# Kernel optimization log

Hardware: AMD Instinct MI355X
Metric: run time of the kernel (lower is better)

## Reference

```python
import jax, jax.numpy as jnp
import numpy as np

B, T, N, C_IN = 2, 12, 50000, 1
H = 16          # hidden = out channels of STConv
KT = 3          # temporal kernel size
E = 800000      # edges (avg degree 16)
NUM_CLASSES = 2


def _temporal_conv(x, wP, bP, wQ, bQ, wR, bR):
    # Gated temporal conv (GLU): relu(P * sigmoid(Q) + R), 'valid' conv over time.
    # x: (B, Tt, N, C); w*: (KT, C, H)
    Tt = x.shape[1]
    def conv(w, b):
        out = b
        for k in range(KT):  # KT=3, tiny unrolled loop
            out = out + jnp.einsum('btnc,co->btno', x[:, k:Tt - KT + 1 + k], w[k])
        return out
    return jax.nn.relu(conv(wP, bP) * jax.nn.sigmoid(conv(wQ, bQ)) + conv(wR, bR))


def _cheb_conv(x, edge_index, edge_weight, w, b):
    # ChebConv K=2, sym normalization, lambda_max=2:
    #   out  = Tx_0 @ W0 + Tx_1 @ W1 + b
    src, dst = edge_index[0], edge_index[1]
    n = x.shape[2]
    deg = jax.ops.segment_sum(edge_weight, src, num_segments=n)
    dis = jnp.where(deg > 0, jax.lax.rsqrt(jnp.maximum(deg, 1e-12)), 0.0)
    norm = -dis[src] * edge_weight * dis[dst]                    # (E,)
    Bc, Tc, _, Hc = x.shape
    xf = jnp.transpose(x, (2, 0, 1, 3)).reshape(n, -1)           # (N, B*T*H)
    agg = jax.ops.segment_sum(norm[:, None] * xf[src], dst, num_segments=n)
    tx1 = jnp.transpose(agg.reshape(n, Bc, Tc, Hc), (1, 2, 0, 3))  # (B, T, N, H)
    return jnp.einsum('btnc,co->btno', x, w[0]) + jnp.einsum('btnc,co->btno', tx1, w[1]) + b


def _forward(x, edge_index, edge_weight,
             tc1_P_w, tc1_P_b, tc1_Q_w, tc1_Q_b, tc1_R_w, tc1_R_b,
             cheb_w, cheb_b,
             tc2_P_w, tc2_P_b, tc2_Q_w, tc2_Q_b, tc2_R_w, tc2_R_b,
             lin_w, lin_b):
    h = _temporal_conv(x, tc1_P_w, tc1_P_b, tc1_Q_w, tc1_Q_b, tc1_R_w, tc1_R_b)  # (B, T-2, N, H)
    h = jax.nn.relu(_cheb_conv(h, edge_index, edge_weight, cheb_w, cheb_b))
    h = _temporal_conv(h, tc2_P_w, tc2_P_b, tc2_Q_w, tc2_Q_b, tc2_R_w, tc2_R_b)  # (B, T-4, N, H)
    h = h.mean(axis=1)                                                            # (B, N, H)
    return h @ lin_w + lin_b                                                      # (B, N, classes)


def setup_inputs() -> dict:
    key = jax.random.key(0)
    ks = jax.random.split(key, 12)
    x = jax.random.normal(ks[0], (B, T, N, C_IN), jnp.float32)
    edge_index = jax.random.randint(ks[1], (2, E), 0, N, dtype=jnp.int32).astype(jnp.int64)
    edge_weight = jax.random.uniform(ks[2], (E,), jnp.float32)

    def conv_w(k, cin, cout):
        s = 1.0 / np.sqrt(cin * KT)
        return jax.random.uniform(k, (KT, cin, cout), jnp.float32, -s, s)

    inp = {'x': x, 'edge_index': edge_index, 'edge_weight': edge_weight}
    for i, name in enumerate(['tc1_P', 'tc1_Q', 'tc1_R']):
        inp[name + '_w'] = conv_w(ks[3 + i], C_IN, H)
        inp[name + '_b'] = jnp.zeros((H,), jnp.float32)
    for i, name in enumerate(['tc2_P', 'tc2_Q', 'tc2_R']):
        inp[name + '_w'] = conv_w(ks[6 + i], H, H)
        inp[name + '_b'] = jnp.zeros((H,), jnp.float32)
    sc = 1.0 / np.sqrt(H)
    inp['cheb_w'] = jax.random.uniform(ks[9], (2, H, H), jnp.float32, -sc, sc)
    inp['cheb_b'] = jnp.zeros((H,), jnp.float32)
    inp['lin_w'] = jax.random.uniform(ks[10], (H, NUM_CLASSES), jnp.float32, -sc, sc)
    inp['lin_b'] = jnp.zeros((NUM_CLASSES,), jnp.float32)
    return inp


def reference(x, edge_index, edge_weight,
              tc1_P_w, tc1_P_b, tc1_Q_w, tc1_Q_b, tc1_R_w, tc1_R_b,
              tc2_P_w, tc2_P_b, tc2_Q_w, tc2_Q_b, tc2_R_w, tc2_R_b,
              cheb_w, cheb_b, lin_w, lin_b):
    return _forward(x, edge_index, edge_weight,
                    tc1_P_w, tc1_P_b, tc1_Q_w, tc1_Q_b, tc1_R_w, tc1_R_b,
                    cheb_w, cheb_b,
                    tc2_P_w, tc2_P_b, tc2_Q_w, tc2_Q_b, tc2_R_w, tc2_R_b,
                    lin_w, lin_b)
```

## Files before the change

kernel.cpp:

```cpp
#include <hip/hip_runtime.h>

typedef unsigned short ushort_t;
typedef unsigned int uint_t;

constexpr int Bb = 2, Tt = 12, Nn = 50000, Hh = 16, Ee = 800000;
constexpr int T1 = 10, T2 = 8;
constexpr int F = 320;
constexpr int NP = 50176;
constexpr int CAP = 64;

#define DEV __device__ __forceinline__

DEV float bf2f(ushort_t u) { return __uint_as_float(((uint_t)u) << 16); }
DEV ushort_t f2bf(float f) {
  uint_t u = __float_as_uint(f);
  u += 0x7fffu + ((u >> 16) & 1u);
  return (ushort_t)(u >> 16);
}
DEV float blo(uint_t u) { return __uint_as_float(u << 16); }
DEV float bhi(uint_t u) { return __uint_as_float(u & 0xffff0000u); }
DEV float sigm(float x) { return 1.0f / (1.0f + __expf(-x)); }

DEV float loadF(const void* p, int j, int isb) {
  return isb ? bf2f(((const ushort_t*)p)[j]) : ((const float*)p)[j];
}
DEV int loadI(const void* p, long long j, int is64) {
  return is64 ? (int)(((const long long*)p)[j]) : ((const int*)p)[j];
}

__global__ void k_wprep(const void* ew, const void* ei,
                        const void* t1Pw, const void* t1Pb,
                        const void* t1Qw, const void* t1Qb,
                        const void* t1Rw, const void* t1Rb,
                        const void* t2Pw, const void* t2Pb,
                        const void* t2Qw, const void* t2Qb,
                        const void* t2Rw, const void* t2Rb,
                        const void* chw, const void* chb,
                        const void* lw, const void* lb,
                        int* flags, float* W, uint_t* zero_base) {
  int gid = blockIdx.x * 256 + threadIdx.x;
  if (gid < 9 * NP) zero_base[gid] = 0u;
  if (blockIdx.x != 0) return;

  __shared__ int sflags[2];
  int tid = threadIdx.x;
  if (tid < 64) {
    int lane = tid;
    const ushort_t* u = (const ushort_t*)ew;
    int cnt = 0;
    for (int j = lane; j < 512; j += 64) cnt += (u[j] < 0x3F80u) ? 1 : 0;
#pragma unroll
    for (int d = 32; d; d >>= 1) cnt += __shfl_xor(cnt, d, 64);
    const int* e32 = (const int*)ei;
    int even_nz = 0, odd_nz = 0;
    for (int j = 2 * lane; j < 256; j += 128) {
      even_nz |= (e32[j] != 0);
      odd_nz |= (e32[j + 1] != 0);
    }
    unsigned long long be = __ballot(even_nz), bo = __ballot(odd_nz);
    if (lane == 0) {
      int f0 = (cnt >= 450) ? 1 : 0;
      int f1 = (bo == 0ull && be != 0ull) ? 1 : 0;
      sflags[0] = f0; sflags[1] = f1;
      flags[0] = f0; flags[1] = f1;
    }
  }
  __syncthreads();
  int isb = sflags[0];
#define CVT(src, off, n) for (int j = tid; j < (n); j += 256) W[(off) + j] = loadF(src, j, isb);
  CVT(t1Pw, 0, 48)   CVT(t1Pb, 48, 16)
  CVT(t1Qw, 64, 48)  CVT(t1Qb, 112, 16)
  CVT(t1Rw, 128, 48) CVT(t1Rb, 176, 16)
  CVT(t2Pw, 192, 768)  CVT(t2Pb, 960, 16)
  CVT(t2Qw, 976, 768)  CVT(t2Qb, 1744, 16)
  CVT(t2Rw, 1760, 768) CVT(t2Rb, 2528, 16)
  CVT(chw, 2544, 512)  CVT(chb, 3056, 16)
  CVT(lw, 3072, 32)    CVT(lb, 3104, 2)
#undef CVT
}

__global__ __launch_bounds__(256) void k_pre(const void* __restrict__ x,
                                             const void* __restrict__ ei,
                                             const void* __restrict__ ew,
                                             const float* __restrict__ W,
                                             const int* __restrict__ flags,
                                             ushort_t* __restrict__ xfh,
                                             float* __restrict__ deg8,
                                             int* __restrict__ cnt,
                                             int2* __restrict__ ecv) {
  int id = blockIdx.x * 256 + threadIdx.x;
  int isb = flags[0];
  if (id < Ee) {
    int is64 = flags[1];
    int s = loadI(ei, id, is64), d = loadI(ei, (long long)Ee + id, is64);
    float w = loadF(ew, id, isb);
    atomicAdd(&deg8[(blockIdx.x & 7) * NP + s], w);
    int pos = atomicAdd(&cnt[d], 1);
    if (pos < CAP) ecv[d * CAP + pos] = make_int2(s, __float_as_int(w));
  }
  if (id < Bb * T1 * Nn) {
    int n = id % Nn;
    int bt = id / Nn;
    int t = bt % T1, b = bt / T1;
    float x0 = loadF(x, (b * Tt + t + 0) * Nn + n, isb);
    float x1 = loadF(x, (b * Tt + t + 1) * Nn + n, isb);
    float x2 = loadF(x, (b * Tt + t + 2) * Nn + n, isb);
    ushort_t g[16];
#pragma unroll
    for (int h = 0; h < 16; ++h) {
      float p = W[48 + h] + x0 * W[0 + h] + x1 * W[16 + h] + x2 * W[32 + h];
      float q = W[112 + h] + x0 * W[64 + h] + x1 * W[80 + h] + x2 * W[96 + h];
      float r = W[176 + h] + x0 * W[128 + h] + x1 * W[144 + h] + x2 * W[160 + h];
      g[h] = f2bf(fmaxf(fmaf(p, sigm(q), r), 0.0f));
    }
    uint_t u[8];
#pragma unroll
    for (int j = 0; j < 8; ++j) u[j] = (uint_t)g[2 * j] | ((uint_t)g[2 * j + 1] << 16);
    uint4* dst = (uint4*)(xfh + (size_t)n * F + t * 32 + b * 16);
    dst[0] = make_uint4(u[0], u[1], u[2], u[3]);
    dst[1] = make_uint4(u[4], u[5], u[6], u[7]);
  }
}

__global__ __launch_bounds__(256) void k_dis(float* __restrict__ deg8) {
  int i = blockIdx.x * 256 + threadIdx.x;
  if (i >= Nn) return;
  float v = 0.0f;
#pragma unroll
  for (int j = 0; j < 8; ++j) v += deg8[j * NP + i];
  deg8[i] = (v > 0.0f) ? (1.0f / sqrtf(fmaxf(v, 1e-12f))) : 0.0f;
}

__global__ __launch_bounds__(256) void k_agg(const int* __restrict__ cnt,
                                             const int2* __restrict__ ecv,
                                             const float* __restrict__ dis,
                                             const uint2* __restrict__ xf2,
                                             const float* __restrict__ W,
                                             ushort_t* __restrict__ h2) {
  __shared__ float sh[4][640];
  int wid = threadIdx.x >> 6;
  int lane = threadIdx.x & 63;
  int gw = blockIdx.x * 4 + wid;
  int deg = min(cnt[gw], CAP);
  int l16 = 64 + (lane & 15);
  float a0 = 0.f, a1 = 0.f, a2 = 0.f, a3 = 0.f;
  float c0 = 0.f, c1 = 0.f, c2 = 0.f, c3 = 0.f;

#define ACC(v, p, q)                                                          \
  a0 = fmaf(v, blo(p.x), a0); a1 = fmaf(v, bhi(p.x), a1);                     \
  a2 = fmaf(v, blo(p.y), a2); a3 = fmaf(v, bhi(p.y), a3);                     \
  c0 = fmaf(v, blo(q.x), c0); c1 = fmaf(v, bhi(q.x), c1);                     \
  c2 = fmaf(v, blo(q.y), c2); c3 = fmaf(v, bhi(q.y), c3);

  int colv = 0; float valv = 0.0f;
  if (lane < deg) {
    int2 t = ecv[gw * CAP + lane];
    colv = t.x * 80;
    valv = __int_as_float(t.y) * dis[t.x];
  }
  int e = 0;
  for (; e + 4 <= deg; e += 4) {
    int r0 = __shfl(colv, e + 0), r1 = __shfl(colv, e + 1);
    int r2 = __shfl(colv, e + 2), r3 = __shfl(colv, e + 3);
    float v0 = __shfl(valv, e + 0), v1 = __shfl(valv, e + 1);
    float v2 = __shfl(valv, e + 2), v3 = __shfl(valv, e + 3);
    uint2 p0 = xf2[r0 + lane], q0 = xf2[r0 + l16];
    uint2 p1 = xf2[r1 + lane], q1 = xf2[r1 + l16];
    uint2 p2 = xf2[r2 + lane], q2 = xf2[r2 + l16];
    uint2 p3 = xf2[r3 + lane], q3 = xf2[r3 + l16];
    ACC(v0, p0, q0) ACC(v1, p1, q1) ACC(v2, p2, q2) ACC(v3, p3, q3)
  }
  for (; e < deg; ++e) {
    int r = __shfl(colv, e);
    float v = __shfl(valv, e);
    uint2 p = xf2[r + lane], q = xf2[r + l16];
    ACC(v, p, q)
  }
#undef ACC

  float nd = -dis[gw];
  float* sa = sh[wid];
  float* sx = sh[wid] + 320;
  const uint2* xrow = xf2 + (size_t)gw * 80;
  uint2 xp = xrow[lane], xq = xrow[l16];
  ((float4*)sa)[lane] = make_float4(a0 * nd, a1 * nd, a2 * nd, a3 * nd);
  ((float4*)sx)[lane] = make_float4(blo(xp.x), bhi(xp.x), blo(xp.y), bhi(xp.y));
  if (lane < 16) {
    ((float4*)sa)[64 + lane] = make_float4(c0 * nd, c1 * nd, c2 * nd, c3 * nd);
    ((float4*)sx)[64 + lane] = make_float4(blo(xq.x), bhi(xq.x), blo(xq.y), bhi(xq.y));
  }
  __builtin_amdgcn_wave_barrier();
  int h = lane & 15;
  float w0[16], w1[16];
#pragma unroll
  for (int c = 0; c < 16; ++c) {
    w0[c] = W[2544 + c * 16 + h];
    w1[c] = W[2800 + c * 16 + h];
  }
  float bias = W[3056 + h];
  ushort_t* orow = h2 + (size_t)gw * F;
#pragma unroll
  for (int j = 0; j < 5; ++j) {
    int base2 = (lane & 48) + 64 * j;
    float o2 = bias;
#pragma unroll
    for (int c = 0; c < 16; ++c)
      o2 = fmaf(sx[base2 + c], w0[c], fmaf(sa[base2 + c], w1[c], o2));
    orow[lane + 64 * j] = f2bf(fmaxf(o2, 0.0f));
  }
}

__global__ __launch_bounds__(256) void k_tc2h(const ushort_t* __restrict__ h2,
                                              const float* __restrict__ W,
                                              float* __restrict__ out) {
  __shared__ float shh[16 * 330];
  __shared__ float sg[16 * 257];
  int tid = threadIdx.x;
  int nb = blockIdx.x * 16;

  for (int i = tid; i < 16 * 40; i += 256) {
    int node = i / 40, j = i % 40;
    uint4 q = ((const uint4*)(h2 + (size_t)(nb + node) * F))[j];
    int t = j >> 2;
    float* dstp = shh + node * 330 + t * 33 + (j & 3) * 8;
    dstp[0] = blo(q.x); dstp[1] = bhi(q.x);
    dstp[2] = blo(q.y); dstp[3] = bhi(q.y);
    dstp[4] = blo(q.z); dstp[5] = bhi(q.z);
    dstp[6] = blo(q.w); dstp[7] = bhi(q.w);
  }
  __syncthreads();

  {
    int node = tid >> 4, pair = tid & 15;
    int b = pair >> 3, t2 = pair & 7;
    const float* base = shh + node * 330 + b * 16;
    float hv[48];
#pragma unroll
    for (int k = 0; k < 3; ++k) {
      const float4* p = (const float4*)(base + (t2 + k) * 33);
      float4 e0 = p[0], e1 = p[1], e2 = p[2], e3 = p[3];
      hv[k * 16 + 0] = e0.x;  hv[k * 16 + 1] = e0.y;
      hv[k * 16 + 2] = e0.z;  hv[k * 16 + 3] = e0.w;
      hv[k * 16 + 4] = e1.x;  hv[k * 16 + 5] = e1.y;
      hv[k * 16 + 6] = e1.z;  hv[k * 16 + 7] = e1.w;
      hv[k * 16 + 8] = e2.x;  hv[k * 16 + 9] = e2.y;
      hv[k * 16 + 10] = e2.z; hv[k * 16 + 11] = e2.w;
      hv[k * 16 + 12] = e3.x; hv[k * 16 + 13] = e3.y;
      hv[k * 16 + 14] = e3.z; hv[k * 16 + 15] = e3.w;
    }
    float P[16], Q[16], R[16];
#pragma unroll
    for (int h = 0; h < 16; ++h) {
      P[h] = W[960 + h];
      Q[h] = W[1744 + h];
      R[h] = W[2528 + h];
    }
#pragma unroll
    for (int k = 0; k < 3; ++k) {
#pragma unroll
      for (int c = 0; c < 16; ++c) {
        float v = hv[k * 16 + c];
        const int wbase = k * 256 + c * 16;
#pragma unroll
        for (int h = 0; h < 16; ++h) {
          P[h] = fmaf(v, W[192 + wbase + h], P[h]);
          Q[h] = fmaf(v, W[976 + wbase + h], Q[h]);
          R[h] = fmaf(v, W[1760 + wbase + h], R[h]);
        }
      }
    }
    float* go = sg + node * 257 + pair * 16;
#pragma unroll
    for (int h = 0; h < 16; ++h)
      go[h] = fmaxf(fmaf(P[h], sigm(Q[h]), R[h]), 0.0f);
  }
  __syncthreads();

  if (tid < 32) {
    int node = tid >> 1, b = tid & 1;
    const float* gp = sg + node * 257 + b * 128;
    float mean[16];
#pragma unroll
    for (int h = 0; h < 16; ++h) mean[h] = 0.0f;
#pragma unroll
    for (int t2 = 0; t2 < T2; ++t2)
#pragma unroll
      for (int h = 0; h < 16; ++h) mean[h] += gp[t2 * 16 + h];
    float o0 = W[3104], o1 = W[3105];
#pragma unroll
    for (int h = 0; h < 16; ++h) {
      float m = mean[h] * 0.125f;
      o0 = fmaf(m, W[3072 + 2 * h], o0);
      o1 = fmaf(m, W[3072 + 2 * h + 1], o1);
    }
    ((float2*)out)[(size_t)b * Nn + nb + node] = make_float2(o0, o1);
  }
}

extern "C" void kernel_launch(void* const* d_in, const int* in_sizes, int n_in,
                              void* d_out, int out_size, void* d_ws, size_t ws_size,
                              hipStream_t stream) {
  (void)in_sizes; (void)n_in; (void)out_size; (void)ws_size;
  const void* x = d_in[0];
  const void* ei = d_in[1];
  const void* ew = d_in[2];

  char* wsb = (char*)d_ws;
  size_t off = 0;
  auto alloc = [&](size_t bytes) -> void* {
    void* p = wsb + off;
    off = (off + bytes + 255) & ~(size_t)255;
    return p;
  };
  int* flags = (int*)alloc(256);
  float* W = (float*)alloc(4096 * 4);
  float* deg8 = (float*)alloc((size_t)8 * NP * 4);
  int* cnt = (int*)alloc((size_t)NP * 4);
  int2* ecv = (int2*)alloc((size_t)Nn * CAP * 8);
  ushort_t* xfh = (ushort_t*)alloc((size_t)Nn * F * 2);
  ushort_t* h2 = (ushort_t*)alloc((size_t)Nn * F * 2);

  int zblk = (9 * NP + 255) / 256;
  k_wprep<<<zblk, 256, 0, stream>>>(
      ew, ei,
      d_in[3], d_in[4], d_in[5], d_in[6], d_in[7], d_in[8],
      d_in[9], d_in[10], d_in[11], d_in[12], d_in[13], d_in[14],
      d_in[15], d_in[16], d_in[17], d_in[18], flags, W, (uint_t*)deg8);

  k_pre<<<(Bb * T1 * Nn + 255) / 256, 256, 0, stream>>>(x, ei, ew, W, flags, xfh, deg8, cnt, ecv);
  k_dis<<<(Nn + 255) / 256, 256, 0, stream>>>(deg8);
  k_agg<<<Nn / 4, 256, 0, stream>>>(cnt, ecv, deg8, (const uint2*)xfh, W, h2);
  k_tc2h<<<Nn / 16, 256, 0, stream>>>(h2, W, (float*)d_out);
}
```

Measured before the change: 333.6 us.

## Stage k_pre outputs in LDS for coalesced stores and pack edges into 32 bits

k_pre now assigns one block to 16 nodes with 320 threads. Each block computes all (b,t) gated outputs for those nodes into shared memory, then writes whole node rows of xfh with contiguous uint4 stores, replacing the strided 32-byte scattered writes. The per-destination edge list is packed into one 32-bit word: the source index in the high 16 bits and a bf16 edge weight in the low 16. This halves ecv traffic in both k_pre and k_agg. The trade-offs are edge weights rounded to bf16 and an added block barrier.

```diff
diff --git a/kernel.cpp b/kernel.cpp
--- a/kernel.cpp
+++ b/kernel.cpp
@@ -79,16 +79,18 @@
 #undef CVT
 }
 
-__global__ __launch_bounds__(256) void k_pre(const void* __restrict__ x,
+__global__ __launch_bounds__(320) void k_pre(const void* __restrict__ x,
                                              const void* __restrict__ ei,
                                              const void* __restrict__ ew,
                                              const float* __restrict__ W,
                                              const int* __restrict__ flags,
-                                             ushort_t* __restrict__ xfh,
+                                             uint_t* __restrict__ xfh,
                                              float* __restrict__ deg8,
                                              int* __restrict__ cnt,
-                                             int2* __restrict__ ecv) {
-  int id = blockIdx.x * 256 + threadIdx.x;
+                                             uint_t* __restrict__ ecv) {
+  __shared__ uint_t sx[16 * 161];
+  int tid = threadIdx.x;
+  int id = blockIdx.x * 320 + tid;
   int isb = flags[0];
   if (id < Ee) {
     int is64 = flags[1];
@@ -96,12 +98,12 @@
     float w = loadF(ew, id, isb);
     atomicAdd(&deg8[(blockIdx.x & 7) * NP + s], w);
     int pos = atomicAdd(&cnt[d], 1);
-    if (pos < CAP) ecv[d * CAP + pos] = make_int2(s, __float_as_int(w));
-  }
-  if (id < Bb * T1 * Nn) {
-    int n = id % Nn;
-    int bt = id / Nn;
-    int t = bt % T1, b = bt / T1;
+    if (pos < CAP) ecv[d * CAP + pos] = ((uint_t)s << 16) | (uint_t)f2bf(w);
+  }
+  {
+    int nlocal = tid & 15, slot = tid >> 4;
+    int t = slot % 10, b = slot / 10;
+    int n = blockIdx.x * 16 + nlocal;
     float x0 = loadF(x, (b * Tt + t + 0) * Nn + n, isb);
     float x1 = loadF(x, (b * Tt + t + 1) * Nn + n, isb);
     float x2 = loadF(x, (b * Tt + t + 2) * Nn + n, isb);
@@ -113,12 +115,19 @@
       float r = W[176 + h] + x0 * W[128 + h] + x1 * W[144 + h] + x2 * W[160 + h];
       g[h] = f2bf(fmaxf(fmaf(p, sigm(q), r), 0.0f));
     }
-    uint_t u[8];
-#pragma unroll
-    for (int j = 0; j < 8; ++j) u[j] = (uint_t)g[2 * j] | ((uint_t)g[2 * j + 1] << 16);
-    uint4* dst = (uint4*)(xfh + (size_t)n * F + t * 32 + b * 16);
-    dst[0] = make_uint4(u[0], u[1], u[2], u[3]);
-    dst[1] = make_uint4(u[4], u[5], u[6], u[7]);
+    uint_t* row = sx + nlocal * 161 + (t * 16 + b * 8);
+#pragma unroll
+    for (int j = 0; j < 8; ++j) row[j] = (uint_t)g[2 * j] | ((uint_t)g[2 * j + 1] << 16);
+  }
+  __syncthreads();
+  uint4* outp = (uint4*)(xfh + (size_t)blockIdx.x * 16 * (F / 2));
+#pragma unroll
+  for (int it = 0; it < 2; ++it) {
+    int i = it * 320 + tid;
+    int f = i * 4;
+    int nr = f / 160, of = f % 160;
+    const uint_t* s = sx + nr * 161 + of;
+    outp[i] = make_uint4(s[0], s[1], s[2], s[3]);
   }
 }
 
@@ -132,7 +141,7 @@
 }
 
 __global__ __launch_bounds__(256) void k_agg(const int* __restrict__ cnt,
-                                             const int2* __restrict__ ecv,
+                                             const uint_t* __restrict__ ecv,
                                              const float* __restrict__ dis,
                                              const uint2* __restrict__ xf2,
                                              const float* __restrict__ W,
@@ -154,9 +163,10 @@
 
   int colv = 0; float valv = 0.0f;
   if (lane < deg) {
-    int2 t = ecv[gw * CAP + lane];
-    colv = t.x * 80;
-    valv = __int_as_float(t.y) * dis[t.x];
+    uint_t t = ecv[gw * CAP + lane];
+    int src = t >> 16;
+    colv = src * 80;
+    valv = bf2f((ushort_t)(t & 0xffffu)) * dis[src];
   }
   int e = 0;
   for (; e + 4 <= deg; e += 4) {
@@ -316,7 +326,7 @@
   float* W = (float*)alloc(4096 * 4);
   float* deg8 = (float*)alloc((size_t)8 * NP * 4);
   int* cnt = (int*)alloc((size_t)NP * 4);
-  int2* ecv = (int2*)alloc((size_t)Nn * CAP * 8);
+  uint_t* ecv = (uint_t*)alloc((size_t)Nn * CAP * 4);
   ushort_t* xfh = (ushort_t*)alloc((size_t)Nn * F * 2);
   ushort_t* h2 = (ushort_t*)alloc((size_t)Nn * F * 2);
 
@@ -327,7 +337,7 @@
       d_in[9], d_in[10], d_in[11], d_in[12], d_in[13], d_in[14],
       d_in[15], d_in[16], d_in[17], d_in[18], flags, W, (uint_t*)deg8);
 
-  k_pre<<<(Bb * T1 * Nn + 255) / 256, 256, 0, stream>>>(x, ei, ew, W, flags, xfh, deg8, cnt, ecv);
+  k_pre<<<Nn / 16, 320, 0, stream>>>(x, ei, ew, W, flags, (uint_t*)xfh, deg8, cnt, ecv);
   k_dis<<<(Nn + 255) / 256, 256, 0, stream>>>(deg8);
   k_agg<<<Nn / 4, 256, 0, stream>>>(cnt, ecv, deg8, (const uint2*)xfh, W, h2);
   k_tc2h<<<Nn / 16, 256, 0, stream>>>(h2, W, (float*)d_out);
```

New measurement: 333.8 us. About the same (+0.1%).
